# Performance work log

Hardware: AMD Instinct MI355X
Metric: run time of the kernel (lower is better)

Reference implementation:

```python
import jax, jax.numpy as jnp
import numpy as np

B, C, H, W = 2, 512, 64, 64
CQ = C // 8  # scale=8

def conv1x1(x, Wt, b):
    # 1x1 conv == per-pixel linear: x [B,Cin,H,W], Wt [Cout,Cin], b [Cout]
    return jnp.einsum('oc,bchw->bohw', Wt, x) + b[None, :, None, None]

def setup_inputs() -> dict:
    key = jax.random.key(0)
    ks = jax.random.split(key, 16)
    s = 0.02
    inp = {
        'x': jax.random.normal(ks[0], (B, C, H, W), jnp.float32),
        'y': jax.random.normal(ks[1], (B, C, H, W), jnp.float32),
        'z': jax.random.normal(ks[2], (B, C, H, W), jnp.float32),
        'Wq': jax.random.normal(ks[3], (CQ, C), jnp.float32) * s,
        'bq': jnp.zeros((CQ,), jnp.float32),
        'Wk1': jax.random.normal(ks[4], (CQ, C), jnp.float32) * s,
        'bk1': jnp.zeros((CQ,), jnp.float32),
        'Wk2': jax.random.normal(ks[5], (CQ, C), jnp.float32) * s,
        'bk2': jnp.zeros((CQ,), jnp.float32),
        'Wk3': jax.random.normal(ks[6], (CQ, C), jnp.float32) * s,
        'bk3': jnp.zeros((CQ,), jnp.float32),
        'Wv': jax.random.normal(ks[7], (C, C), jnp.float32) * s,
        'bv': jnp.zeros((C,), jnp.float32),
        'Wl': jax.random.normal(ks[8], (C, C), jnp.float32) * s,
        'bl': jnp.zeros((C,), jnp.float32),
        'gamma': jnp.full((1,), 0.1, jnp.float32),  # torch init is 0; nonzero for meaningful output
    }
    return inp

def reference(x, y, z, Wq, bq, Wk1, bk1, Wk2, bk2, Wk3, bk3, Wv, bv, Wl, bl, gamma):
    b, c, h, w = x.shape
    n = h * w
    Q = conv1x1(x, Wq, bq).reshape(b, -1, n)    # [B,CQ,N]
    K = conv1x1(x, Wk1, bk1).reshape(b, -1, n)
    yK = conv1x1(y, Wk2, bk2).reshape(b, -1, n)
    zK = conv1x1(z, Wk3, bk3).reshape(b, -1, n)
    V = conv1x1(x, Wv, bv).reshape(b, -1, n)    # [B,C,N]

    def branch(Kb):
        scores = jnp.einsum('bcn,bcm->bnm', Q, Kb)        # [B,N,N]
        attn = jax.nn.softmax(scores, axis=-1)
        return jnp.einsum('bmn,bcm->bcn', attn, V)        # [B,C,N]

    att = branch(K) + branch(yK) + branch(zK)
    att = att.reshape(b, c, h, w)
    att = conv1x1(att, Wl, bl)
    return x + gamma[0] * att
```

## Files before the change

### kernel.cpp

```cpp
#include <hip/hip_runtime.h>


typedef __attribute__((ext_vector_type(8))) short short8;
typedef __attribute__((ext_vector_type(4))) float f32x4;
#define MFMA_BF16(a,b,c) __builtin_amdgcn_mfma_f32_16x16x32_bf16((a),(b),(c),0,0,0)

#define NN 4096
#define CC 512
#define CQd 64

#define OFF_WQ   ((size_t)0)
#define OFF_WK1  ((size_t)65536)
#define OFF_WK2  ((size_t)131072)
#define OFF_WK3  ((size_t)196608)
#define OFF_WLB  ((size_t)262144)
#define OFF_WVT  ((size_t)786432)
#define OFF_WU   ((size_t)1310720)
#define OFF_BU   ((size_t)1835008)
#define OFF_QT   ((size_t)1837056)
#define OFF_K1T  ((size_t)2885632)
#define OFF_K2T  ((size_t)3934208)
#define OFF_K3T  ((size_t)4982784)
#define OFF_U    ((size_t)6031360)
#define OFF_Z    ((size_t)14419968)
#define OFF_PT   ((size_t)14813184)
#define OFF_XT   ((size_t)56756224)
#define OFF_PART ((size_t)81922048)

__device__ __forceinline__ unsigned short f2bf(float f) {
    unsigned int u = __float_as_uint(f);
    u = u + 0x7FFFu + ((u >> 16) & 1u);
    return (unsigned short)(u >> 16);
}
__device__ __forceinline__ ushort4 pack4(float a, float b, float c, float d) {
    return make_ushort4(f2bf(a), f2bf(b), f2bf(c), f2bf(d));
}
__device__ __forceinline__ float bf2f(unsigned short u) {
    return __uint_as_float(((unsigned int)u) << 16);
}
__device__ __forceinline__ void gll16(const void* g, void* l) {
    __builtin_amdgcn_global_load_lds(
        (const __attribute__((address_space(1))) void*)g,
        (__attribute__((address_space(3))) void*)l, 16, 0, 0);
}

__global__ __launch_bounds__(256) void cast_k(
    const float* __restrict__ s0, const float* __restrict__ s1, const float* __restrict__ s2,
    const float* __restrict__ s3, const float* __restrict__ s4, char* __restrict__ ws)
{
    const int y = blockIdx.y;
    const float* src = (y==0)?s0:(y==1)?s1:(y==2)?s2:(y==3)?s3:s4;
    const size_t off = (y==0)?OFF_WQ:(y==1)?OFF_WK1:(y==2)?OFF_WK2:(y==3)?OFF_WK3:OFF_WLB;
    ushort* dst = (ushort*)(ws + off);
    const int size = (y < 4) ? (CQd*CC) : (CC*CC);
    const int idx = (blockIdx.x * 256 + threadIdx.x) * 4;
    if (idx < size) {
        const float4 v = *(const float4*)(src + idx);
        *(ushort4*)(dst + idx) = pack4(v.x, v.y, v.z, v.w);
    }
}

__global__ __launch_bounds__(256) void wvt_k(const float* __restrict__ Wv, ushort* __restrict__ WvT)
{
    const int i0 = blockIdx.x * 64, c0 = blockIdx.y * 64;
    __shared__ float tile[64][65];
    const int t = threadIdx.x, tr = t >> 6, tc = t & 63;
#pragma unroll
    for (int p = 0; p < 16; ++p) {
        const int r = p * 4 + tr;
        tile[r][tc] = Wv[(size_t)(c0 + r) * CC + i0 + tc];
    }
    __syncthreads();
#pragma unroll
    for (int p = 0; p < 16; ++p) {
        const int ir = p * 4 + tr;
        WvT[(size_t)(i0 + ir) * CC + c0 + tc] = f2bf(tile[tc][ir]);
    }
}

__global__ __launch_bounds__(256) void transpose_k(
    const float* __restrict__ x, const float* __restrict__ y, const float* __restrict__ z,
    ushort* __restrict__ xt_base)
{
    const int zi = blockIdx.z;
    const int s = zi >> 1, b = zi & 1;
    const float* src = ((s==0) ? x : (s==1) ? y : z) + (size_t)b * CC * NN;
    ushort* dst = xt_base + (size_t)s * 2 * NN * CC + (size_t)b * NN * CC;
    const int n0 = blockIdx.x * 64, c0 = blockIdx.y * 64;
    __shared__ float tile[64][65];
    const int t = threadIdx.x, tr = t >> 6, tc = t & 63;
#pragma unroll
    for (int p = 0; p < 16; ++p) {
        const int r = p * 4 + tr;
        tile[r][tc] = src[(size_t)(c0 + r) * NN + n0 + tc];
    }
    __syncthreads();
#pragma unroll
    for (int p = 0; p < 16; ++p) {
        const int nr = p * 4 + tr;
        dst[(size_t)(n0 + nr) * CC + c0 + tc] = f2bf(tile[tc][nr]);
    }
}

__global__ __launch_bounds__(256) void bu_k(
    const float* __restrict__ Wl, const float* __restrict__ bv, float* __restrict__ bU)
{
    const int o0 = blockIdx.x * 64;
    const int t = threadIdx.x, r = t >> 2, seg = t & 3;
    const float* wp = Wl + (size_t)(o0 + r) * CC + seg * 128;
    const float* vp = bv + seg * 128;
    float s = 0.f;
#pragma unroll 8
    for (int c = 0; c < 128; c += 4) {
        const float4 wv = *(const float4*)(wp + c);
        const float4 bb = *(const float4*)(vp + c);
        s += wv.x*bb.x + wv.y*bb.y + wv.z*bb.z + wv.w*bb.w;
    }
    __shared__ float red[64][4];
    red[r][seg] = s;
    __syncthreads();
    if (t < 64) bU[o0 + t] = red[t][0] + red[t][1] + red[t][2] + red[t][3];
}

__global__ __launch_bounds__(256) void wlwv_k(
    const ushort* __restrict__ WlB, const ushort* __restrict__ WvT, ushort* __restrict__ WU)
{
    const int n0 = blockIdx.x * 64, o0 = blockIdx.y * 64;
    const int t = threadIdx.x, w = t >> 6, lane = t & 63;
    const int m = lane & 15, q = lane >> 4;
    const int ow = o0 + (w >> 1) * 32, nw = n0 + (w & 1) * 32;

    const ushort* Ap = WlB + (size_t)(ow + m) * CC + q * 8;
    const ushort* Bp = WvT + (size_t)(nw + m) * CC + q * 8;

    f32x4 acc[2][2];
#pragma unroll
    for (int i = 0; i < 2; ++i)
#pragma unroll
        for (int j = 0; j < 2; ++j) acc[i][j] = (f32x4)(0.f);

    short8 ab[2][2], bb[2][2];
    auto ld = [&](int s, int k) {
#pragma unroll
        for (int f = 0; f < 2; ++f) {
            ab[s][f] = *(const short8*)(Ap + (size_t)f * 16 * CC + k);
            bb[s][f] = *(const short8*)(Bp + (size_t)f * 16 * CC + k);
        }
    };
    auto comp = [&](int s) {
#pragma unroll
        for (int mf = 0; mf < 2; ++mf)
#pragma unroll
            for (int nf = 0; nf < 2; ++nf)
                acc[mf][nf] = MFMA_BF16(ab[s][mf], bb[s][nf], acc[mf][nf]);
    };
    ld(0, 0); ld(1, 32);
    for (int i = 0; i < 16; i += 2) {
        comp(0); ld(0, ((i + 2 < 16) ? (i + 2) : 15) * 32);
        comp(1); ld(1, ((i + 3 < 16) ? (i + 3) : 15) * 32);
    }
#pragma unroll
    for (int mf = 0; mf < 2; ++mf)
#pragma unroll
        for (int nf = 0; nf < 2; ++nf) {
            const int col = nw + nf * 16 + m;
#pragma unroll
            for (int rr = 0; rr < 4; ++rr)
                WU[(size_t)(ow + mf * 16 + q * 4 + rr) * CC + col] = f2bf(acc[mf][nf][rr]);
        }
}

__global__ __launch_bounds__(256) void projU_k(
    const char* __restrict__ ws,
    const float* __restrict__ bq, const float* __restrict__ bk1,
    const float* __restrict__ bk2, const float* __restrict__ bk3)
{
    const int rt = blockIdx.y, b = blockIdx.z, n0 = blockIdx.x * 128;
    const int t = threadIdx.x, w = t >> 6, lane = t & 63;
    const int m = lane & 15, q = lane >> 4;
    const int nw = n0 + w * 32;

    const ushort* W;
    const float* bias;
    int sel;
    ushort* dst;
    if (rt < 4) {
        W    = (const ushort*)(ws + ((rt==0)?OFF_WQ:(rt==1)?OFF_WK1:(rt==2)?OFF_WK2:OFF_WK3));
        bias = (rt==0)?bq:(rt==1)?bk1:(rt==2)?bk2:bk3;
        sel  = (rt==2) ? 1 : (rt==3) ? 2 : 0;
        dst  = (ushort*)(ws + ((rt==0)?OFF_QT:(rt==1)?OFF_K1T:(rt==2)?OFF_K2T:OFF_K3T))
               + (size_t)b * NN * CQd;
    } else {
        W    = (const ushort*)(ws + OFF_WU) + (size_t)(rt - 4) * 64 * CC;
        bias = (const float*)(ws + OFF_BU) + (rt - 4) * 64;
        sel  = 0;
        dst  = (ushort*)(ws + OFF_U) + (size_t)b * CC * NN + (size_t)(rt - 4) * 64 * NN;
    }
    const ushort* Bt = (const ushort*)(ws + OFF_XT) + ((size_t)sel * 2 + b) * NN * CC;

    const ushort* Ap = W + (size_t)m * CC + q * 8;
    const ushort* Bp = Bt + (size_t)(nw + m) * CC + q * 8;

    f32x4 acc[4][2];
#pragma unroll
    for (int i = 0; i < 4; ++i)
#pragma unroll
        for (int j = 0; j < 2; ++j) acc[i][j] = (f32x4)(0.f);

    short8 ab[2][4], bb[2][2];
    auto ld = [&](int s, int k) {
#pragma unroll
        for (int f = 0; f < 4; ++f)
            ab[s][f] = *(const short8*)(Ap + (size_t)f * 16 * CC + k);
#pragma unroll
        for (int g = 0; g < 2; ++g)
            bb[s][g] = *(const short8*)(Bp + (size_t)g * 16 * CC + k);
    };
    auto comp = [&](int s) {
#pragma unroll
        for (int mf = 0; mf < 4; ++mf)
#pragma unroll
            for (int nf = 0; nf < 2; ++nf)
                acc[mf][nf] = MFMA_BF16(ab[s][mf], bb[s][nf], acc[mf][nf]);
    };
    ld(0, 0); ld(1, 32);
    for (int i = 0; i < 16; i += 2) {
        comp(0); ld(0, ((i + 2 < 16) ? (i + 2) : 15) * 32);
        comp(1); ld(1, ((i + 3 < 16) ? (i + 3) : 15) * 32);
    }

    if (rt < 4) {
#pragma unroll
        for (int mf = 0; mf < 4; ++mf) {
            const int r0 = mf * 16 + q * 4;
            const float b0 = bias[r0], b1 = bias[r0+1], b2 = bias[r0+2], b3 = bias[r0+3];
#pragma unroll
            for (int nf = 0; nf < 2; ++nf) {
                const f32x4 v = acc[mf][nf];
                *(ushort4*)(dst + (size_t)(nw + nf*16 + m) * CQd + r0) =
                    pack4(v[0]+b0, v[1]+b1, v[2]+b2, v[3]+b3);
            }
        }
    } else {
#pragma unroll
        for (int mf = 0; mf < 4; ++mf) {
            const int r0 = mf * 16 + q * 4;
#pragma unroll
            for (int rr = 0; rr < 4; ++rr) {
                const float bo = bias[r0 + rr];
#pragma unroll
                for (int nf = 0; nf < 2; ++nf)
                    dst[(size_t)(r0 + rr) * NN + nw + nf*16 + m] = f2bf(acc[mf][nf][rr] + bo);
            }
        }
    }
}

__global__ __launch_bounds__(256) void rowstats_k(
    const ushort* __restrict__ Qt, const ushort* __restrict__ K1t,
    const ushort* __restrict__ K2t, const ushort* __restrict__ K3t,
    float* __restrict__ Zpart)
{
    const int it = blockIdx.x, jq = blockIdx.y, b = blockIdx.z;
    const int t = threadIdx.x, w = t >> 6, lane = t & 63;
    const int m = lane & 15, quad = lane >> 4;
    const int i0 = it * 64 + w * 16;

    const ushort* Qp = Qt + (size_t)b * NN * CQd;
    const ushort* Kp[3] = { K1t + (size_t)b * NN * CQd,
                            K2t + (size_t)b * NN * CQd,
                            K3t + (size_t)b * NN * CQd };

    const short8 a0 = *(const short8*)(Qp + (size_t)(i0 + m) * CQd + quad * 8);
    const short8 a1 = *(const short8*)(Qp + (size_t)(i0 + m) * CQd + 32 + quad * 8);

    float z[3][4];
#pragma unroll
    for (int br = 0; br < 3; ++br)
#pragma unroll
        for (int r = 0; r < 4; ++r) z[br][r] = 0.f;

    for (int jt = 0; jt < 16; ++jt) {
        const int jb = jq * 1024 + jt * 64;
#pragma unroll
        for (int br = 0; br < 3; ++br) {
#pragma unroll
            for (int nf = 0; nf < 4; ++nf) {
                const ushort* kp = Kp[br] + (size_t)(jb + nf * 16 + m) * CQd + quad * 8;
                const short8 b0 = *(const short8*)kp;
                const short8 b1 = *(const short8*)(kp + 32);
                f32x4 sf = MFMA_BF16(a0, b0, (f32x4)(0.f));
                sf = MFMA_BF16(a1, b1, sf);
                z[br][0] += __expf(sf[0]);
                z[br][1] += __expf(sf[1]);
                z[br][2] += __expf(sf[2]);
                z[br][3] += __expf(sf[3]);
            }
        }
    }
#pragma unroll
    for (int br = 0; br < 3; ++br)
#pragma unroll
        for (int r = 0; r < 4; ++r) {
            float v = z[br][r];
            v += __shfl_xor(v, 1);
            v += __shfl_xor(v, 2);
            v += __shfl_xor(v, 4);
            v += __shfl_xor(v, 8);
            if (m == 0)
                Zpart[(((size_t)jq * 3 + br) * 2 + b) * NN + i0 + quad * 4 + r] = v;
        }
}

__global__ __launch_bounds__(256) void pmat_k(
    const ushort* __restrict__ Qt, const ushort* __restrict__ K1t,
    const ushort* __restrict__ K2t, const ushort* __restrict__ K3t,
    const float* __restrict__ Zpart, ushort* __restrict__ Pt)
{
    const int j0 = blockIdx.x * 128, i0 = blockIdx.y * 64, b = blockIdx.z;
    const int t = threadIdx.x, w = t >> 6, lane = t & 63;
    const int m = lane & 15, quad = lane >> 4;
    const int jw = j0 + w * 32;

    __shared__ float zinv[3][64];
    __shared__ ushort pbuf[4][32][72];
    if (t < 192) {
        const int br = t >> 6, il = t & 63;
        float s = 0.f;
#pragma unroll
        for (int p = 0; p < 4; ++p)
            s += Zpart[(((size_t)p * 3 + br) * 2 + b) * NN + i0 + il];
        zinv[br][il] = 1.f / s;
    }
    __syncthreads();

    const ushort* Qp = Qt + (size_t)b * NN * CQd;
    const ushort* Kp[3] = { K1t + (size_t)b * NN * CQd,
                            K2t + (size_t)b * NN * CQd,
                            K3t + (size_t)b * NN * CQd };
    short8 a[4][2];
#pragma unroll
    for (int mf = 0; mf < 4; ++mf) {
        const ushort* ap = Qp + (size_t)(i0 + mf * 16 + m) * CQd + quad * 8;
        a[mf][0] = *(const short8*)ap;
        a[mf][1] = *(const short8*)(ap + 32);
    }

    f32x4 pacc[4][2];
#pragma unroll
    for (int mf = 0; mf < 4; ++mf)
#pragma unroll
        for (int nf = 0; nf < 2; ++nf) pacc[mf][nf] = (f32x4)(0.f);

#pragma unroll
    for (int br = 0; br < 3; ++br) {
        float rz[4][4];
#pragma unroll
        for (int mf = 0; mf < 4; ++mf)
#pragma unroll
            for (int r = 0; r < 4; ++r)
                rz[mf][r] = zinv[br][mf * 16 + quad * 4 + r];
#pragma unroll
        for (int nf = 0; nf < 2; ++nf) {
            const ushort* kp = Kp[br] + (size_t)(jw + nf * 16 + m) * CQd + quad * 8;
            const short8 b0 = *(const short8*)kp;
            const short8 b1 = *(const short8*)(kp + 32);
#pragma unroll
            for (int mf = 0; mf < 4; ++mf) {
                f32x4 sf = MFMA_BF16(a[mf][0], b0, (f32x4)(0.f));
                sf = MFMA_BF16(a[mf][1], b1, sf);
                pacc[mf][nf][0] += __expf(sf[0]) * rz[mf][0];
                pacc[mf][nf][1] += __expf(sf[1]) * rz[mf][1];
                pacc[mf][nf][2] += __expf(sf[2]) * rz[mf][2];
                pacc[mf][nf][3] += __expf(sf[3]) * rz[mf][3];
            }
        }
    }

#pragma unroll
    for (int mf = 0; mf < 4; ++mf)
#pragma unroll
        for (int nf = 0; nf < 2; ++nf) {
            const f32x4 v = pacc[mf][nf];
            *(ushort4*)&pbuf[w][nf * 16 + m][mf * 16 + quad * 4] = pack4(v[0], v[1], v[2], v[3]);
        }
    ushort* Pb = Pt + (size_t)b * NN * NN;
#pragma unroll
    for (int p = 0; p < 4; ++p) {
        const int row = p * 8 + (lane >> 3);
        const int c16 = lane & 7;
        const uint4 v = *(const uint4*)&pbuf[w][row][c16 * 8];
        *(uint4*)(Pb + (size_t)(jw + row) * NN + i0 + c16 * 8) = v;
    }
}

__global__ __launch_bounds__(256) void av_k(
    const ushort* __restrict__ U, const ushort* __restrict__ Pt,
    ushort* __restrict__ Part)
{
    const int t = threadIdx.x, w = t >> 6, lane = t & 63;
    const int m = lane & 15, q = lane >> 4;
    const int zz = blockIdx.z;
    const int b = zz >> 1, h = zz & 1;
    const int j0 = blockIdx.x * 128;
    const int c0 = blockIdx.y * 128;
    const int k00 = h * 2048;

    __shared__ ushort As[128][64];
    __shared__ ushort Bs[128][64];

    const ushort* Ub = U + (size_t)b * CC * NN;
    const ushort* Pb = Pt + (size_t)b * NN * NN;

    const int srow = w * 32 + (lane >> 3);
    const int scol = (lane & 7) * 8;
    const ushort* gA = Ub + (size_t)(c0 + srow) * NN + k00 + scol;
    const ushort* gB = Pb + (size_t)(j0 + srow) * NN + k00 + scol;

    const int cw = (w >> 1) * 64, jw = (w & 1) * 64;

    f32x4 acc[4][4];
#pragma unroll
    for (int i = 0; i < 4; ++i)
#pragma unroll
        for (int j = 0; j < 4; ++j) acc[i][j] = (f32x4)(0.f);

    for (int k0 = 0; k0 < 2048; k0 += 64) {
        __syncthreads();
#pragma unroll
        for (int i2 = 0; i2 < 4; ++i2) {
            gll16(gA + (size_t)i2 * 8 * NN + k0, &As[w * 32 + i2 * 8][0]);
            gll16(gB + (size_t)i2 * 8 * NN + k0, &Bs[w * 32 + i2 * 8][0]);
        }
        __syncthreads();
#pragma unroll
        for (int kk = 0; kk < 2; ++kk) {
            short8 af[4], bf[4];
#pragma unroll
            for (int f = 0; f < 4; ++f) {
                af[f] = *(const short8*)&As[cw + f * 16 + m][kk * 32 + q * 8];
                bf[f] = *(const short8*)&Bs[jw + f * 16 + m][kk * 32 + q * 8];
            }
#pragma unroll
            for (int mf = 0; mf < 4; ++mf)
#pragma unroll
                for (int nf = 0; nf < 4; ++nf)
                    acc[mf][nf] = MFMA_BF16(af[mf], bf[nf], acc[mf][nf]);
        }
    }

    ushort* Pp = Part + ((size_t)h * 2 + b) * CC * NN;
#pragma unroll
    for (int mf = 0; mf < 4; ++mf) {
        const int r0 = c0 + cw + mf * 16 + q * 4;
#pragma unroll
        for (int nf = 0; nf < 4; ++nf) {
            const int col = j0 + jw + nf * 16 + m;
            const f32x4 v = acc[mf][nf];
            Pp[(size_t)(r0 + 0) * NN + col] = f2bf(v[0]);
            Pp[(size_t)(r0 + 1) * NN + col] = f2bf(v[1]);
            Pp[(size_t)(r0 + 2) * NN + col] = f2bf(v[2]);
            Pp[(size_t)(r0 + 3) * NN + col] = f2bf(v[3]);
        }
    }
}

__global__ __launch_bounds__(256) void fin_k(
    const ushort* __restrict__ Part, const float* __restrict__ x,
    const float* __restrict__ bl, const float* __restrict__ gam,
    float* __restrict__ out)
{
    const int row = blockIdx.x;
    const int b = row >> 9, c = row & 511;
    const int col = blockIdx.y * 1024 + threadIdx.x * 4;
    const float g = gam[0];
    const float bo = bl[c];
    const size_t base = ((size_t)b * CC + c) * NN + col;
    const ushort4 p0 = *(const ushort4*)(Part + ((size_t)b * CC + c) * NN + col);
    const ushort4 p1 = *(const ushort4*)(Part + ((size_t)(2 + b) * CC + c) * NN + col);
    const float4 xv = *(const float4*)(x + base);
    float4 o;
    o.x = xv.x + g * (bf2f(p0.x) + bf2f(p1.x) + bo);
    o.y = xv.y + g * (bf2f(p0.y) + bf2f(p1.y) + bo);
    o.z = xv.z + g * (bf2f(p0.z) + bf2f(p1.z) + bo);
    o.w = xv.w + g * (bf2f(p0.w) + bf2f(p1.w) + bo);
    *(float4*)(out + base) = o;
}

extern "C" void kernel_launch(void* const* d_in, const int* in_sizes, int n_in,
                              void* d_out, int out_size, void* d_ws, size_t ws_size,
                              hipStream_t stream)
{
    (void)in_sizes; (void)n_in; (void)out_size; (void)ws_size;

    const float* xp  = (const float*)d_in[0];
    const float* yp  = (const float*)d_in[1];
    const float* zp  = (const float*)d_in[2];
    const float* Wq  = (const float*)d_in[3];
    const float* bq  = (const float*)d_in[4];
    const float* Wk1 = (const float*)d_in[5];
    const float* bk1 = (const float*)d_in[6];
    const float* Wk2 = (const float*)d_in[7];
    const float* bk2 = (const float*)d_in[8];
    const float* Wk3 = (const float*)d_in[9];
    const float* bk3 = (const float*)d_in[10];
    const float* Wv  = (const float*)d_in[11];
    const float* bv  = (const float*)d_in[12];
    const float* Wl  = (const float*)d_in[13];
    const float* bl  = (const float*)d_in[14];
    const float* gam = (const float*)d_in[15];
    float* out = (float*)d_out;

    char* ws = (char*)d_ws;
    ushort* WVT = (ushort*)(ws + OFF_WVT);
    ushort* WU  = (ushort*)(ws + OFF_WU);
    float*  BU  = (float*)(ws + OFF_BU);
    const ushort* QT  = (const ushort*)(ws + OFF_QT);
    const ushort* K1T = (const ushort*)(ws + OFF_K1T);
    const ushort* K2T = (const ushort*)(ws + OFF_K2T);
    const ushort* K3T = (const ushort*)(ws + OFF_K3T);
    const ushort* Ub  = (const ushort*)(ws + OFF_U);
    float*  ZP  = (float*)(ws + OFF_Z);
    ushort* PT  = (ushort*)(ws + OFF_PT);
    ushort* XT  = (ushort*)(ws + OFF_XT);
    ushort* PRT = (ushort*)(ws + OFF_PART);

    cast_k<<<dim3(256, 5), 256, 0, stream>>>(Wq, Wk1, Wk2, Wk3, Wl, ws);
    wvt_k<<<dim3(8, 8), 256, 0, stream>>>(Wv, WVT);
    transpose_k<<<dim3(64, 8, 6), 256, 0, stream>>>(xp, yp, zp, XT);
    bu_k<<<dim3(8), 256, 0, stream>>>(Wl, bv, BU);
    wlwv_k<<<dim3(8, 8), 256, 0, stream>>>((const ushort*)(ws + OFF_WLB), WVT, WU);
    projU_k<<<dim3(32, 12, 2), 256, 0, stream>>>(ws, bq, bk1, bk2, bk3);
    rowstats_k<<<dim3(64, 4, 2), 256, 0, stream>>>(QT, K1T, K2T, K3T, ZP);
    pmat_k<<<dim3(32, 64, 2), 256, 0, stream>>>(QT, K1T, K2T, K3T, ZP, PT);
    av_k<<<dim3(32, 4, 4), 256, 0, stream>>>(Ub, PT, PRT);
    fin_k<<<dim3(1024, 4), 256, 0, stream>>>(PRT, xp, bl, gam, out);
}
```

Baseline: 364.4 us.

## Fold log2e into Q weights, retile rowstats for reuse, prefetch K fragments

Q weights and bias are prescaled by log2(e) so softmax exponentials can use exp2f instead of __expf, which drops a multiply per element. The rowstats kernel is retiled so each wave covers 64 query rows and 32 key columns, reusing its Q fragments across four MFMA row tiles. K fragments are double-buffered in registers to overlap loads with MFMA work, and the same prefetch is added to pmat. The partial-sum buffer grows from 4 to 16 slices, so the workspace offsets move and pmat sums more partials. Register pressure rises in both kernels.

```diff
diff --git a/kernel.cpp b/kernel.cpp
--- a/kernel.cpp
+++ b/kernel.cpp
@@ -8,6 +8,7 @@
 #define NN 4096
 #define CC 512
 #define CQd 64
+#define LOG2E 1.4426950408889634f
 
 #define OFF_WQ   ((size_t)0)
 #define OFF_WK1  ((size_t)65536)
@@ -23,9 +24,9 @@
 #define OFF_K3T  ((size_t)4982784)
 #define OFF_U    ((size_t)6031360)
 #define OFF_Z    ((size_t)14419968)
-#define OFF_PT   ((size_t)14813184)
-#define OFF_XT   ((size_t)56756224)
-#define OFF_PART ((size_t)81922048)
+#define OFF_PT   ((size_t)15992832)
+#define OFF_XT   ((size_t)57935872)
+#define OFF_PART ((size_t)83101696)
 
 __device__ __forceinline__ unsigned short f2bf(float f) {
     unsigned int u = __float_as_uint(f);
@@ -53,10 +54,11 @@
     const size_t off = (y==0)?OFF_WQ:(y==1)?OFF_WK1:(y==2)?OFF_WK2:(y==3)?OFF_WK3:OFF_WLB;
     ushort* dst = (ushort*)(ws + off);
     const int size = (y < 4) ? (CQd*CC) : (CC*CC);
+    const float sc = (y == 0) ? LOG2E : 1.0f;
     const int idx = (blockIdx.x * 256 + threadIdx.x) * 4;
     if (idx < size) {
         const float4 v = *(const float4*)(src + idx);
-        *(ushort4*)(dst + idx) = pack4(v.x, v.y, v.z, v.w);
+        *(ushort4*)(dst + idx) = pack4(v.x*sc, v.y*sc, v.z*sc, v.w*sc);
     }
 }
 
@@ -197,6 +199,7 @@
         dst  = (ushort*)(ws + OFF_U) + (size_t)b * CC * NN + (size_t)(rt - 4) * 64 * NN;
     }
     const ushort* Bt = (const ushort*)(ws + OFF_XT) + ((size_t)sel * 2 + b) * NN * CC;
+    const float bsc = (rt == 0) ? LOG2E : 1.0f;
 
     const ushort* Ap = W + (size_t)m * CC + q * 8;
     const ushort* Bp = Bt + (size_t)(nw + m) * CC + q * 8;
@@ -233,7 +236,8 @@
 #pragma unroll
         for (int mf = 0; mf < 4; ++mf) {
             const int r0 = mf * 16 + q * 4;
-            const float b0 = bias[r0], b1 = bias[r0+1], b2 = bias[r0+2], b3 = bias[r0+3];
+            const float b0 = bias[r0]*bsc, b1 = bias[r0+1]*bsc,
+                        b2 = bias[r0+2]*bsc, b3 = bias[r0+3]*bsc;
 #pragma unroll
             for (int nf = 0; nf < 2; ++nf) {
                 const f32x4 v = acc[mf][nf];
@@ -264,52 +268,79 @@
     const int it = blockIdx.x, jq = blockIdx.y, b = blockIdx.z;
     const int t = threadIdx.x, w = t >> 6, lane = t & 63;
     const int m = lane & 15, quad = lane >> 4;
-    const int i0 = it * 64 + w * 16;
-
-    const ushort* Qp = Qt + (size_t)b * NN * CQd;
-    const ushort* Kp[3] = { K1t + (size_t)b * NN * CQd,
-                            K2t + (size_t)b * NN * CQd,
-                            K3t + (size_t)b * NN * CQd };
-
-    const short8 a0 = *(const short8*)(Qp + (size_t)(i0 + m) * CQd + quad * 8);
-    const short8 a1 = *(const short8*)(Qp + (size_t)(i0 + m) * CQd + 32 + quad * 8);
-
-    float z[3][4];
+    const int i0 = it * 64;
+    const int jbase = jq * 1024 + w * 32;
+
+    const ushort* Qp  = Qt  + (size_t)b * NN * CQd;
+    const ushort* Kp0 = K1t + (size_t)b * NN * CQd;
+    const ushort* Kp1 = K2t + (size_t)b * NN * CQd;
+    const ushort* Kp2 = K3t + (size_t)b * NN * CQd;
+
+    short8 a[4][2];
+#pragma unroll
+    for (int mf = 0; mf < 4; ++mf) {
+        const ushort* ap = Qp + (size_t)(i0 + mf * 16 + m) * CQd + quad * 8;
+        a[mf][0] = *(const short8*)ap;
+        a[mf][1] = *(const short8*)(ap + 32);
+    }
+
+    float z[3][4][4];
 #pragma unroll
     for (int br = 0; br < 3; ++br)
 #pragma unroll
-        for (int r = 0; r < 4; ++r) z[br][r] = 0.f;
-
-    for (int jt = 0; jt < 16; ++jt) {
-        const int jb = jq * 1024 + jt * 64;
+        for (int mf = 0; mf < 4; ++mf)
+#pragma unroll
+            for (int r = 0; r < 4; ++r) z[br][mf][r] = 0.f;
+
+    short8 kb[2][2][2];
+    auto ldk = [&](int slot, int s, int br) {
+        const ushort* Kb = (br == 0) ? Kp0 : (br == 1) ? Kp1 : Kp2;
+#pragma unroll
+        for (int nf = 0; nf < 2; ++nf) {
+            const ushort* kp = Kb + (size_t)(jbase + s * 128 + nf * 16 + m) * CQd + quad * 8;
+            kb[slot][nf][0] = *(const short8*)kp;
+            kb[slot][nf][1] = *(const short8*)(kp + 32);
+        }
+    };
+
+    ldk(0, 0, 0);
+    int slot = 0;
+    for (int s8 = 0; s8 < 8; ++s8) {
 #pragma unroll
         for (int br = 0; br < 3; ++br) {
-#pragma unroll
-            for (int nf = 0; nf < 4; ++nf) {
-                const ushort* kp = Kp[br] + (size_t)(jb + nf * 16 + m) * CQd + quad * 8;
-                const short8 b0 = *(const short8*)kp;
-                const short8 b1 = *(const short8*)(kp + 32);
-                f32x4 sf = MFMA_BF16(a0, b0, (f32x4)(0.f));
-                sf = MFMA_BF16(a1, b1, sf);
-                z[br][0] += __expf(sf[0]);
-                z[br][1] += __expf(sf[1]);
-                z[br][2] += __expf(sf[2]);
-                z[br][3] += __expf(sf[3]);
+            const int ns = (br == 2) ? ((s8 < 7) ? s8 + 1 : 7) : s8;
+            const int nb = (br == 2) ? 0 : br + 1;
+            ldk(slot ^ 1, ns, nb);
+#pragma unroll
+            for (int nf = 0; nf < 2; ++nf)
+#pragma unroll
+                for (int mf = 0; mf < 4; ++mf) {
+                    f32x4 sf = MFMA_BF16(a[mf][0], kb[slot][nf][0], (f32x4)(0.f));
+                    sf = MFMA_BF16(a[mf][1], kb[slot][nf][1], sf);
+                    z[br][mf][0] += exp2f(sf[0]);
+                    z[br][mf][1] += exp2f(sf[1]);
+                    z[br][mf][2] += exp2f(sf[2]);
+                    z[br][mf][3] += exp2f(sf[3]);
+                }
+            slot ^= 1;
+        }
+    }
+
+    const int p = jq * 4 + w;
+#pragma unroll
+    for (int br = 0; br < 3; ++br)
+#pragma unroll
+        for (int mf = 0; mf < 4; ++mf)
+#pragma unroll
+            for (int r = 0; r < 4; ++r) {
+                float v = z[br][mf][r];
+                v += __shfl_xor(v, 1);
+                v += __shfl_xor(v, 2);
+                v += __shfl_xor(v, 4);
+                v += __shfl_xor(v, 8);
+                if (m == 0)
+                    Zpart[(((size_t)p * 3 + br) * 2 + b) * NN + i0 + mf * 16 + quad * 4 + r] = v;
             }
-        }
-    }
-#pragma unroll
-    for (int br = 0; br < 3; ++br)
-#pragma unroll
-        for (int r = 0; r < 4; ++r) {
-            float v = z[br][r];
-            v += __shfl_xor(v, 1);
-            v += __shfl_xor(v, 2);
-            v += __shfl_xor(v, 4);
-            v += __shfl_xor(v, 8);
-            if (m == 0)
-                Zpart[(((size_t)jq * 3 + br) * 2 + b) * NN + i0 + quad * 4 + r] = v;
-        }
 }
 
 __global__ __launch_bounds__(256) void pmat_k(
@@ -328,16 +359,17 @@
         const int br = t >> 6, il = t & 63;
         float s = 0.f;
 #pragma unroll
-        for (int p = 0; p < 4; ++p)
+        for (int p = 0; p < 16; ++p)
             s += Zpart[(((size_t)p * 3 + br) * 2 + b) * NN + i0 + il];
         zinv[br][il] = 1.f / s;
     }
     __syncthreads();
 
-    const ushort* Qp = Qt + (size_t)b * NN * CQd;
-    const ushort* Kp[3] = { K1t + (size_t)b * NN * CQd,
-                            K2t + (size_t)b * NN * CQd,
-                            K3t + (size_t)b * NN * CQd };
+    const ushort* Qp  = Qt  + (size_t)b * NN * CQd;
+    const ushort* Kp0 = K1t + (size_t)b * NN * CQd;
+    const ushort* Kp1 = K2t + (size_t)b * NN * CQd;
+    const ushort* Kp2 = K3t + (size_t)b * NN * CQd;
+
     short8 a[4][2];
 #pragma unroll
     for (int mf = 0; mf < 4; ++mf) {
@@ -352,29 +384,39 @@
 #pragma unroll
         for (int nf = 0; nf < 2; ++nf) pacc[mf][nf] = (f32x4)(0.f);
 
-#pragma unroll
-    for (int br = 0; br < 3; ++br) {
-        float rz[4][4];
-#pragma unroll
-        for (int mf = 0; mf < 4; ++mf)
-#pragma unroll
-            for (int r = 0; r < 4; ++r)
-                rz[mf][r] = zinv[br][mf * 16 + quad * 4 + r];
-#pragma unroll
-        for (int nf = 0; nf < 2; ++nf) {
-            const ushort* kp = Kp[br] + (size_t)(jw + nf * 16 + m) * CQd + quad * 8;
-            const short8 b0 = *(const short8*)kp;
-            const short8 b1 = *(const short8*)(kp + 32);
-#pragma unroll
-            for (int mf = 0; mf < 4; ++mf) {
-                f32x4 sf = MFMA_BF16(a[mf][0], b0, (f32x4)(0.f));
-                sf = MFMA_BF16(a[mf][1], b1, sf);
-                pacc[mf][nf][0] += __expf(sf[0]) * rz[mf][0];
-                pacc[mf][nf][1] += __expf(sf[1]) * rz[mf][1];
-                pacc[mf][nf][2] += __expf(sf[2]) * rz[mf][2];
-                pacc[mf][nf][3] += __expf(sf[3]) * rz[mf][3];
-            }
-        }
+    short8 kb[2][2];
+    auto ldk = [&](int slot, int u) {
+        const int br = u >> 1, nf = u & 1;
+        const ushort* Kb = (br == 0) ? Kp0 : (br == 1) ? Kp1 : Kp2;
+        const ushort* kp = Kb + (size_t)(jw + nf * 16 + m) * CQd + quad * 8;
+        kb[slot][0] = *(const short8*)kp;
+        kb[slot][1] = *(const short8*)(kp + 32);
+    };
+
+    ldk(0, 0);
+    int slot = 0;
+    float rz[4][4];
+#pragma unroll
+    for (int u = 0; u < 6; ++u) {
+        ldk(slot ^ 1, (u < 5) ? u + 1 : 5);
+        const int br = u >> 1, nf = u & 1;
+        if (nf == 0) {
+#pragma unroll
+            for (int mf = 0; mf < 4; ++mf)
+#pragma unroll
+                for (int r = 0; r < 4; ++r)
+                    rz[mf][r] = zinv[br][mf * 16 + quad * 4 + r];
+        }
+#pragma unroll
+        for (int mf = 0; mf < 4; ++mf) {
+            f32x4 sf = MFMA_BF16(a[mf][0], kb[slot][0], (f32x4)(0.f));
+            sf = MFMA_BF16(a[mf][1], kb[slot][1], sf);
+            pacc[mf][nf][0] += exp2f(sf[0]) * rz[mf][0];
+            pacc[mf][nf][1] += exp2f(sf[1]) * rz[mf][1];
+            pacc[mf][nf][2] += exp2f(sf[2]) * rz[mf][2];
+            pacc[mf][nf][3] += exp2f(sf[3]) * rz[mf][3];
+        }
+        slot ^= 1;
     }
 
 #pragma unroll
```

Result: slower. 376.4 us (+3.3%).
